# Performance work log

Measured on AMD Instinct MI355X. Metric: run time of the kernel, lower is better.

## Reference

```python
import jax, jax.numpy as jnp
import numpy as np
from jax import lax

H = 250  # hidden size of all LSTM layers


def _lstm_layer(x, Wih, Whh, bih, bhh):
    """Single-layer LSTM over time-major x [T, in], batch=1 folded away.
    PyTorch gate order: i, f, g, o. Returns hidden states [T, H]."""
    b = bih + bhh
    # Precompute input projections for all timesteps (parallel GEMM)
    xW = x @ Wih.T + b  # [T, 4H]

    def step(carry, xw_t):
        h, c = carry
        gates = xw_t + h @ Whh.T  # [4H]
        i, f, g, o = jnp.split(gates, 4)
        i = jax.nn.sigmoid(i)
        f = jax.nn.sigmoid(f)
        g = jnp.tanh(g)
        o = jax.nn.sigmoid(o)
        c = f * c + i * g
        h = o * jnp.tanh(c)
        return (h, c), h

    h0 = jnp.zeros((Whh.shape[1],), x.dtype)
    (_, _), hs = lax.scan(step, (h0, h0), xW)
    return hs  # [T, H]


def setup_inputs() -> dict:
    key = jax.random.key(0)
    ks = jax.random.split(key, 16)
    T, D = 8192, 1
    s = 1.0 / np.sqrt(H)  # PyTorch default uniform(-1/sqrt(H), 1/sqrt(H))
    u = lambda k, shape: jax.random.uniform(k, shape, jnp.float32, -s, s)
    inp = {
        "input_seq": jax.random.normal(ks[0], (T, D), jnp.float32),
        # lstm (2 layers), layer 0: input_size=1
        "Wih0": u(ks[1], (4 * H, D)), "Whh0": u(ks[2], (4 * H, H)),
        "bih0": u(ks[3], (4 * H,)), "bhh0": u(ks[4], (4 * H,)),
        # lstm layer 1: input=H
        "Wih1": u(ks[5], (4 * H, H)), "Whh1": u(ks[6], (4 * H, H)),
        "bih1": u(ks[7], (4 * H,)), "bhh1": u(ks[8], (4 * H,)),
        # lstm_1 (1 layer): input=H
        "Wih2": u(ks[9], (4 * H, H)), "Whh2": u(ks[10], (4 * H, H)),
        "bih2": u(ks[11], (4 * H,)), "bhh2": u(ks[12], (4 * H,)),
        # final linear H -> 1
        "Wl": u(ks[13], (1, H)), "bl": u(ks[14], (1,)),
    }
    return inp


def reference(input_seq, Wih0, Whh0, bih0, bhh0, Wih1, Whh1, bih1, bhh1,
              Wih2, Whh2, bih2, bhh2, Wl, bl):
    T = input_seq.shape[0]
    x = input_seq.reshape(T, -1)            # [T, 1] (batch=1 squeezed)
    h0 = _lstm_layer(x, Wih0, Whh0, bih0, bhh0)   # stacked LSTM layer 0
    h1 = _lstm_layer(h0, Wih1, Whh1, bih1, bhh1)  # layer 1 (dropout=0.2 inactive at eval)
    h2 = _lstm_layer(h1, Wih2, Whh2, bih2, bhh2)  # second LSTM module
    preds = h2 @ Wl.T + bl                  # [T, 1]
    return preds[-1]                        # [1]
```

## Files before the change

kernel.cpp:

```cpp
#include <hip/hip_runtime.h>
#include <cstdint>

#define HDIM 250
#define GDIM 1000
#define CH   64
#define PP   4
#define HRING 4
#define XRING 4
#define RPAD 1024
#define NTH  1024

#define LQ_N 8
#define LDSW_BYTES (LQ_N * NTH * 16)
#define HSEG 144
#define HBUF (4 * HSEG)
#define HB_BASE LDSW_BYTES
#define RED_BASE (HB_BASE + 2 * HBUF)
#define SMEM_BYTES (RED_BASE + 1024)

typedef _Float16 f16x2 __attribute__((ext_vector_type(2)));

__device__ __forceinline__ float fdot2u(uint32_t w, uint32_t h, float acc) {
#if defined(__has_builtin) && __has_builtin(__builtin_amdgcn_fdot2)
  return __builtin_amdgcn_fdot2(__builtin_bit_cast(f16x2, w),
                                __builtin_bit_cast(f16x2, h), acc, false);
#else
  f16x2 wv = __builtin_bit_cast(f16x2, w), hv = __builtin_bit_cast(f16x2, h);
  return acc + (float)wv[0] * (float)hv[0] + (float)wv[1] * (float)hv[1];
#endif
}

__device__ __forceinline__ uint32_t pkh2(float a, float b) {
  f16x2 p; p[0] = (_Float16)a; p[1] = (_Float16)b;
  return __builtin_bit_cast(uint32_t, p);
}

__device__ __forceinline__ uint4 pack8q(const float* rp, int c0) {
  float c[8];
#pragma unroll
  for (int u = 0; u < 8; ++u) {
    int col = c0 + u;
    c[u] = (rp && col < HDIM) ? rp[col] : 0.f;
  }
  uint4 r;
  r.x = pkh2(c[0], c[1]); r.y = pkh2(c[2], c[3]);
  r.z = pkh2(c[4], c[5]); r.w = pkh2(c[6], c[7]);
  return r;
}

__device__ __forceinline__ float rcpf_(float x) {
#if defined(__has_builtin) && __has_builtin(__builtin_amdgcn_rcpf)
  return __builtin_amdgcn_rcpf(x);
#else
  return 1.f / x;
#endif
}
__device__ __forceinline__ float sigm(float x) {
  return rcpf_(1.f + exp2f(-1.44269504088896341f * x));
}
__device__ __forceinline__ float tanh_(float x) {
  float e = exp2f(2.88539008177792681f * x);
  return 1.f - 2.f * rcpf_(e + 1.f);
}

template <int CTRL>
__device__ __forceinline__ float dppq(float v) {
  return __builtin_bit_cast(
      float, __builtin_amdgcn_update_dpp(0, __builtin_bit_cast(int, v), CTRL,
                                         0xF, 0xF, true));
}

__device__ __forceinline__ void step_barrier() {
  asm volatile("s_waitcnt lgkmcnt(0)\n\ts_barrier" ::: "memory");
}

#define F_HCNT(F, li)     (F)[(li)]
#define F_XWCON(F, li)    (F)[2 + (li)]
#define F_HDONE(F, li, p) (F)[4 + (li) * PP + (p)]
#define F_XWRDY(F, li, c) (F)[16 + (li) * 128 + (c)]

__device__ __forceinline__ int aload(int* p) {
  return __hip_atomic_load(p, __ATOMIC_RELAXED, __HIP_MEMORY_SCOPE_AGENT);
}
__device__ __forceinline__ void arel(int* p, int v) {
  __hip_atomic_store(p, v, __ATOMIC_RELEASE, __HIP_MEMORY_SCOPE_AGENT);
}
__device__ __forceinline__ void acq_fence() {
  __builtin_amdgcn_fence(__ATOMIC_ACQUIRE, "agent");
}
__device__ __forceinline__ void spin_ge(int* p, int tgt) {
  unsigned n = 0;
  while (aload(p) < tgt) {
    __builtin_amdgcn_s_sleep(2);
    if (++n > 200000000u) return;
  }
}

__global__ void lstm_init(const float* __restrict__ Wih1, const float* __restrict__ bih1,
                          const float* __restrict__ bhh1, const float* __restrict__ Wih2,
                          const float* __restrict__ bih2, const float* __restrict__ bhh2,
                          float* __restrict__ WT, float* __restrict__ BV) {
  int idx = blockIdx.x * blockDim.x + threadIdx.x;
  int stride = gridDim.x * blockDim.x;
  for (int i = idx; i < 2 * HDIM * RPAD; i += stride) {
    int li = i / (HDIM * RPAD);
    int rem = i - li * HDIM * RPAD;
    int j = rem / RPAD, r = rem - j * RPAD;
    const float* W = li ? Wih2 : Wih1;
    WT[i] = (r < GDIM) ? W[r * HDIM + j] : 0.f;
  }
  for (int i = idx; i < 2 * RPAD; i += stride) {
    int li = i >> 10, r = i & 1023;
    const float* bi = li ? bih2 : bih1;
    const float* bh = li ? bhh2 : bhh1;
    BV[i] = (r < GDIM) ? bi[r] + bh[r] : 0.f;
  }
}

__global__ void __launch_bounds__(NTH) lstm_main(
    const float* __restrict__ x, const float* __restrict__ Wih0,
    const float* __restrict__ bih0, const float* __restrict__ bhh0,
    const float* __restrict__ Whh0, const float* __restrict__ Whh1,
    const float* __restrict__ Whh2, const float* __restrict__ Wl,
    const float* __restrict__ bl, int* __restrict__ F,
    const float* __restrict__ WT, const float* __restrict__ BV,
    float* __restrict__ hRing, float* __restrict__ xwRing,
    float* __restrict__ out, int T) {
  __shared__ __align__(16) char smem[SMEM_BYTES];
  const int tid = threadIdx.x;
  const int bid = blockIdx.x;
  const int NC = T / CH;

  if (bid < 3) {
    const int L = bid;
    const int u = tid >> 2, sl = tid & 3;
    const bool uok = (u < HDIM);
    const int r_abs = sl * HDIM + u;

    const float* Whh = (L == 0) ? Whh0 : (L == 1) ? Whh1 : Whh2;
    char* lw = smem + tid * 16;
#define LWADDR(lq) (lw + (size_t)(lq) * (NTH * 16))
#define ROWP(r) (uok ? (Whh + ((size_t)(r) * HDIM + u) * HDIM) : (const float*)nullptr)

    uint4 w00, w01, w02, w03, w04, w05;
    uint4 w10, w11, w12, w13, w14, w15;
    uint4 w20, w21, w22, w23, w24, w25;
    uint4 w30, w31, w32, w33, w34, w35;
#define INITROW(r)                                          \
  w##r##0 = pack8q(ROWP(r), sl * 64 + 0);                   \
  w##r##1 = pack8q(ROWP(r), sl * 64 + 8);                   \
  w##r##2 = pack8q(ROWP(r), sl * 64 + 16);                  \
  w##r##3 = pack8q(ROWP(r), sl * 64 + 24);                  \
  w##r##4 = pack8q(ROWP(r), sl * 64 + 32);                  \
  w##r##5 = pack8q(ROWP(r), sl * 64 + 40);                  \
  *(uint4*)LWADDR(2 * (r)) = pack8q(ROWP(r), sl * 64 + 48); \
  *(uint4*)LWADDR(2 * (r) + 1) = pack8q(ROWP(r), sl * 64 + 56);
    INITROW(0) INITROW(1) INITROW(2) INITROW(3)

    float w0_ = 0.f, b0_ = 0.f;
    if (L == 0 && uok) {
      w0_ = Wih0[r_abs];
      b0_ = bih0[r_abs] + bhh0[r_abs];
    }

    for (int i = tid; i < (2 * HBUF) / 4; i += NTH)
      *(uint32_t*)(smem + HB_BASE + 4 * i) = 0u;
    __syncthreads();

    const float* xwBase = xwRing + (size_t)(L > 0 ? L - 1 : 0) * XRING * CH * RPAD;
    float* hBase = hRing + (size_t)L * HRING * CH * HDIM;
    float c_st = 0.f, h_last = 0.f;

    for (int tt = 0; tt < T; ++tt) {
      const int tc = tt & (CH - 1);
      const int c = tt >> 6;
      if (tc == 0) {
        if (tid == 0) {
          if (L > 0) spin_ge(&F_XWRDY(F, L - 1, c), 1);
          if (L < 2 && c >= HRING) {
            int cc = c - HRING;
            spin_ge(&F_HDONE(F, L, cc % PP), cc + 1);
          }
          acq_fence();
        }
        __syncthreads();
      }

      float xw = 0.f;
      if (uok) {
        if (L == 0) {
          xw = fmaf(x[tt], w0_, b0_);
        } else {
          const float* xp = xwBase + (size_t)(c & (XRING - 1)) * CH * RPAD +
                            (size_t)tc * RPAD;
          xw = xp[r_abs];
        }
      }

      const char* hb = smem + HB_BASE + (tt & 1) * HBUF + sl * HSEG;
      float a0 = 0.f, a1 = 0.f, a2 = 0.f, a3 = 0.f;
#define FD4(W_, H_, A_)                \
  A_ = fdot2u((W_).x, (H_).x, A_);     \
  A_ = fdot2u((W_).y, (H_).y, A_);     \
  A_ = fdot2u((W_).z, (H_).z, A_);     \
  A_ = fdot2u((W_).w, (H_).w, A_);
#define DOTK(k)                                      \
  {                                                  \
    const uint4 hq = *(const uint4*)(hb + (k) * 16); \
    FD4(w0##k, hq, a0)                               \
    FD4(w1##k, hq, a1)                               \
    FD4(w2##k, hq, a2)                               \
    FD4(w3##k, hq, a3)                               \
  }
      DOTK(0) DOTK(1) DOTK(2) DOTK(3) DOTK(4) DOTK(5)
      {
        const uint4 hq = *(const uint4*)(hb + 96);
        uint4 q;
        q = *(const uint4*)LWADDR(0); FD4(q, hq, a0)
        q = *(const uint4*)LWADDR(2); FD4(q, hq, a1)
        q = *(const uint4*)LWADDR(4); FD4(q, hq, a2)
        q = *(const uint4*)LWADDR(6); FD4(q, hq, a3)
      }
      {
        const uint4 hq = *(const uint4*)(hb + 112);
        uint4 q;
        q = *(const uint4*)LWADDR(1); FD4(q, hq, a0)
        q = *(const uint4*)LWADDR(3); FD4(q, hq, a1)
        q = *(const uint4*)LWADDR(5); FD4(q, hq, a2)
        q = *(const uint4*)LWADDR(7); FD4(q, hq, a3)
      }

      a0 += (sl == 0) ? xw : 0.f;
      a1 += (sl == 1) ? xw : 0.f;
      a2 += (sl == 2) ? xw : 0.f;
      a3 += (sl == 3) ? xw : 0.f;
      a0 += dppq<0xB1>(a0); a0 += dppq<0x4E>(a0);
      a1 += dppq<0xB1>(a1); a1 += dppq<0x4E>(a1);
      a2 += dppq<0xB1>(a2); a2 += dppq<0x4E>(a2);
      a3 += dppq<0xB1>(a3); a3 += dppq<0x4E>(a3);

      float ii = sigm(a0), ff = sigm(a1), tg = tanh_(a2), oo = sigm(a3);
      c_st = ff * c_st + ii * tg;
      float hn = oo * tanh_(c_st);
      h_last = hn;

      if (sl == 0 && uok) {
        char* hw = smem + HB_BASE + ((tt + 1) & 1) * HBUF + (u >> 6) * HSEG +
                   (u & 63) * 2;
        *(_Float16*)hw = (_Float16)hn;
        if (L < 2)
          hBase[(size_t)(c & (HRING - 1)) * CH * HDIM + (size_t)tc * HDIM + u] = hn;
      }

      if (tc == CH - 1) {
        __syncthreads();
        if (tid == 0) {
          if (L < 2) arel(&F_HCNT(F, L), c + 1);
          if (L > 0) arel(&F_XWCON(F, L - 1), c + 1);
        }
      } else {
        step_barrier();
      }
    }

    if (L == 2) {
      float* red = (float*)(smem + RED_BASE);
      if (sl == 0 && uok) red[u] = h_last;
      __syncthreads();
      if (tid == 0) {
        float s = bl[0];
        for (int j = 0; j < HDIM; ++j) s += red[j] * Wl[j];
        out[0] = s;
      }
    }
  } else {
    const int li = (bid - 3) / PP;
    const int p = (bid - 3) % PP;
    float* ldsH = (float*)smem;
    const int lane = tid & 63, wid = tid >> 6;
    const float* WTl = WT + (size_t)li * HDIM * RPAD;
    const float* BVl = BV + (size_t)li * RPAD;

    for (int c = p; c < NC; c += PP) {
      if (tid == 0) {
        spin_ge(&F_HCNT(F, li), c + 1);
        if (c >= XRING) spin_ge(&F_XWCON(F, li), c - XRING + 1);
        acq_fence();
      }
      __syncthreads();
      const float* hsrc = hRing + (size_t)li * HRING * CH * HDIM +
                          (size_t)(c & (HRING - 1)) * CH * HDIM;
      for (int t = wid; t < CH; t += 16)
        for (int j = lane; j < HDIM; j += 64)
          ldsH[t * 257 + j] = hsrc[t * HDIM + j];
      __syncthreads();
      if (tid == 0) arel(&F_HDONE(F, li, p), c + 1);

      float* xdst = xwRing + (size_t)li * XRING * CH * RPAD +
                    (size_t)(c & (XRING - 1)) * CH * RPAD;
      const int rb0 = wid * 64;
      for (int grpq = 0; grpq < 8; ++grpq) {
        const int rb = rb0 + grpq * 8;
        float acc[8];
#pragma unroll
        for (int uq = 0; uq < 8; ++uq) acc[uq] = 0.f;
        const float* wp = WTl + rb;
        float4 wa4 = *(const float4*)(wp);
        float4 wb4 = *(const float4*)(wp + 4);
        for (int j = 0; j < HDIM; ++j) {
          int jn = (j + 1 < HDIM) ? j + 1 : HDIM - 1;
          float4 na = *(const float4*)(wp + (size_t)jn * RPAD);
          float4 nb = *(const float4*)(wp + (size_t)jn * RPAD + 4);
          float hj = ldsH[lane * 257 + j];
          acc[0] = fmaf(wa4.x, hj, acc[0]); acc[1] = fmaf(wa4.y, hj, acc[1]);
          acc[2] = fmaf(wa4.z, hj, acc[2]); acc[3] = fmaf(wa4.w, hj, acc[3]);
          acc[4] = fmaf(wb4.x, hj, acc[4]); acc[5] = fmaf(wb4.y, hj, acc[5]);
          acc[6] = fmaf(wb4.z, hj, acc[6]); acc[7] = fmaf(wb4.w, hj, acc[7]);
          wa4 = na; wb4 = nb;
        }
#pragma unroll
        for (int uq = 0; uq < 8; ++uq) {
          int r = rb + uq;
          if (r < GDIM) xdst[(size_t)lane * RPAD + r] = acc[uq] + BVl[r];
        }
      }
      __syncthreads();
      if (tid == 0) arel(&F_XWRDY(F, li, c), 1);
    }
  }
}

extern "C" void kernel_launch(void* const* d_in, const int* in_sizes, int n_in,
                              void* d_out, int out_size, void* d_ws, size_t ws_size,
                              hipStream_t stream) {
  const float* x    = (const float*)d_in[0];
  const float* Wih0 = (const float*)d_in[1];
  const float* Whh0 = (const float*)d_in[2];
  const float* bih0 = (const float*)d_in[3];
  const float* bhh0 = (const float*)d_in[4];
  const float* Wih1 = (const float*)d_in[5];
  const float* Whh1 = (const float*)d_in[6];
  const float* bih1 = (const float*)d_in[7];
  const float* bhh1 = (const float*)d_in[8];
  const float* Wih2 = (const float*)d_in[9];
  const float* Whh2 = (const float*)d_in[10];
  const float* bih2 = (const float*)d_in[11];
  const float* bhh2 = (const float*)d_in[12];
  const float* Wl   = (const float*)d_in[13];
  const float* bl   = (const float*)d_in[14];
  const int T = in_sizes[0];

  char* ws = (char*)d_ws;
  int*   F   = (int*)ws;
  float* WT  = (float*)(ws + 4096);
  float* BV  = (float*)(ws + 4096 + 2048000);
  float* hR  = (float*)(ws + 4096 + 2048000 + 8192);
  float* xwR = (float*)(ws + 4096 + 2048000 + 8192 + 512000);

  hipMemsetAsync(F, 0, 4096, stream);
  lstm_init<<<256, 256, 0, stream>>>(Wih1, bih1, bhh1, Wih2, bih2, bhh2, WT, BV);
  lstm_main<<<3 + 2 * PP, NTH, 0, stream>>>(
      x, Wih0, bih0, bhh0, Whh0, Whh1, Whh2, Wl, bl, F, WT, BV, hR, xwR,
      (float*)d_out, T);
}
```

Measured before the change: 19.82 ms.

## Split each recurrent LSTM layer across four workgroups with cross-block hidden-state exchange

Each recurrent layer now runs on four workgroups, each owning a slice of about 64 hidden units with all four gate rows, instead of one workgroup per layer. This cuts per-step dot-product work and register and LDS weight storage per block. Hidden states are exchanged every timestep through global memory with per-block flags and spin-waits, and gates are gathered with ds_swizzle. The change trades per-step compute for a global-memory round trip and cross-CU synchronisation on the serial critical path, so latency could grow.

Measured after the change: 27.68 ms. +39.7%, slower.

```diff
diff --git a/kernel.cpp b/kernel.cpp
--- a/kernel.cpp
+++ b/kernel.cpp
@@ -5,18 +5,17 @@
 #define GDIM 1000
 #define CH   64
 #define PP   4
+#define NW   4
 #define HRING 4
 #define XRING 4
 #define RPAD 1024
 #define NTH  1024
 
-#define LQ_N 8
-#define LDSW_BYTES (LQ_N * NTH * 16)
 #define HSEG 144
 #define HBUF (4 * HSEG)
-#define HB_BASE LDSW_BYTES
+#define HB_BASE 32768
 #define RED_BASE (HB_BASE + 2 * HBUF)
-#define SMEM_BYTES (RED_BASE + 1024)
+#define SMEM_BYTES 92160
 
 typedef _Float16 f16x2 __attribute__((ext_vector_type(2)));
 
@@ -69,15 +68,21 @@
       float, __builtin_amdgcn_update_dpp(0, __builtin_bit_cast(int, v), CTRL,
                                          0xF, 0xF, true));
 }
+template <int IMM>
+__device__ __forceinline__ float swz(float v) {
+  return __builtin_bit_cast(
+      float, __builtin_amdgcn_ds_swizzle(__builtin_bit_cast(int, v), IMM));
+}
 
 __device__ __forceinline__ void step_barrier() {
   asm volatile("s_waitcnt lgkmcnt(0)\n\ts_barrier" ::: "memory");
 }
 
-#define F_HCNT(F, li)     (F)[(li)]
-#define F_XWCON(F, li)    (F)[2 + (li)]
-#define F_HDONE(F, li, p) (F)[4 + (li) * PP + (p)]
-#define F_XWRDY(F, li, c) (F)[16 + (li) * 128 + (c)]
+#define F_HCNTW(F, li, w)  (F)[(li) * 4 + (w)]
+#define F_XWCONW(F, li, w) (F)[8 + (li) * 4 + (w)]
+#define F_HDONE(F, li, p)  (F)[16 + (li) * 4 + (p)]
+#define F_XWRDY(F, li, c)  (F)[32 + (li) * 128 + (c)]
+#define F_HXC(F, L, w)     (F)[512 + (L) * 4 + (w)]
 
 __device__ __forceinline__ int aload(int* p) {
   return __hip_atomic_load(p, __ATOMIC_RELAXED, __HIP_MEMORY_SCOPE_AGENT);
@@ -92,7 +97,7 @@
   unsigned n = 0;
   while (aload(p) < tgt) {
     __builtin_amdgcn_s_sleep(2);
-    if (++n > 200000000u) return;
+    if (++n > 100000000u) return;
   }
 }
 
@@ -122,7 +127,7 @@
     const float* __restrict__ bih0, const float* __restrict__ bhh0,
     const float* __restrict__ Whh0, const float* __restrict__ Whh1,
     const float* __restrict__ Whh2, const float* __restrict__ Wl,
-    const float* __restrict__ bl, int* __restrict__ F,
+    const float* __restrict__ bl, int* __restrict__ F, float* __restrict__ hx,
     const float* __restrict__ WT, const float* __restrict__ BV,
     float* __restrict__ hRing, float* __restrict__ xwRing,
     float* __restrict__ out, int T) {
@@ -131,31 +136,30 @@
   const int bid = blockIdx.x;
   const int NC = T / CH;
 
-  if (bid < 3) {
-    const int L = bid;
-    const int u = tid >> 2, sl = tid & 3;
-    const bool uok = (u < HDIM);
-    const int r_abs = sl * HDIM + u;
+  if (bid < 12) {
+    const int L = bid >> 2, w = bid & 3;
+    const int sl = tid & 3;
+    const int gate = (tid >> 2) & 3;
+    const int lu = tid >> 4;
+    const int UW = (w < 3) ? 64 : 58;
+    const int u_glob = w * 64 + lu;
+    const bool uok = (lu < UW);
+    const bool lead = ((tid & 15) == 0) && uok;
+    const int r_abs = gate * HDIM + u_glob;
 
     const float* Whh = (L == 0) ? Whh0 : (L == 1) ? Whh1 : Whh2;
+    const float* rp = uok ? (Whh + (size_t)r_abs * HDIM) : (const float*)nullptr;
     char* lw = smem + tid * 16;
-#define LWADDR(lq) (lw + (size_t)(lq) * (NTH * 16))
-#define ROWP(r) (uok ? (Whh + ((size_t)(r) * HDIM + u) * HDIM) : (const float*)nullptr)
-
-    uint4 w00, w01, w02, w03, w04, w05;
-    uint4 w10, w11, w12, w13, w14, w15;
-    uint4 w20, w21, w22, w23, w24, w25;
-    uint4 w30, w31, w32, w33, w34, w35;
-#define INITROW(r)                                          \
-  w##r##0 = pack8q(ROWP(r), sl * 64 + 0);                   \
-  w##r##1 = pack8q(ROWP(r), sl * 64 + 8);                   \
-  w##r##2 = pack8q(ROWP(r), sl * 64 + 16);                  \
-  w##r##3 = pack8q(ROWP(r), sl * 64 + 24);                  \
-  w##r##4 = pack8q(ROWP(r), sl * 64 + 32);                  \
-  w##r##5 = pack8q(ROWP(r), sl * 64 + 40);                  \
-  *(uint4*)LWADDR(2 * (r)) = pack8q(ROWP(r), sl * 64 + 48); \
-  *(uint4*)LWADDR(2 * (r) + 1) = pack8q(ROWP(r), sl * 64 + 56);
-    INITROW(0) INITROW(1) INITROW(2) INITROW(3)
+#define LW(q) (lw + (size_t)(q) * (NTH * 16))
+
+    uint4 q0 = pack8q(rp, sl * 64 + 0);
+    uint4 q1 = pack8q(rp, sl * 64 + 8);
+    uint4 q2 = pack8q(rp, sl * 64 + 16);
+    uint4 q3 = pack8q(rp, sl * 64 + 24);
+    uint4 q4 = pack8q(rp, sl * 64 + 32);
+    uint4 q5 = pack8q(rp, sl * 64 + 40);
+    *(uint4*)LW(0) = pack8q(rp, sl * 64 + 48);
+    *(uint4*)LW(1) = pack8q(rp, sl * 64 + 56);
 
     float w0_ = 0.f, b0_ = 0.f;
     if (L == 0 && uok) {
@@ -163,17 +167,28 @@
       b0_ = bih0[r_abs] + bhh0[r_abs];
     }
 
+    const int lt = tid - 768;
+    int cw = -1, li2 = 0;
+    bool loader = false;
+    if (lt >= 0 && lt < 96) {
+      int idx = lt >> 5;
+      li2 = lt & 31;
+      cw = idx + (idx >= w ? 1 : 0);
+      loader = li2 < ((cw == 3) ? 29 : 32);
+    }
+
     for (int i = tid; i < (2 * HBUF) / 4; i += NTH)
       *(uint32_t*)(smem + HB_BASE + 4 * i) = 0u;
     __syncthreads();
 
     const float* xwBase = xwRing + (size_t)(L > 0 ? L - 1 : 0) * XRING * CH * RPAD;
     float* hBase = hRing + (size_t)L * HRING * CH * HDIM;
-    float c_st = 0.f, h_last = 0.f;
+    float c_st = 0.f;
 
     for (int tt = 0; tt < T; ++tt) {
       const int tc = tt & (CH - 1);
       const int c = tt >> 6;
+      const int p = tt & 1, ns = p ^ 1;
       if (tc == 0) {
         if (tid == 0) {
           if (L > 0) spin_ge(&F_XWRDY(F, L - 1, c), 1);
@@ -197,85 +212,86 @@
         }
       }
 
-      const char* hb = smem + HB_BASE + (tt & 1) * HBUF + sl * HSEG;
-      float a0 = 0.f, a1 = 0.f, a2 = 0.f, a3 = 0.f;
-#define FD4(W_, H_, A_)                \
-  A_ = fdot2u((W_).x, (H_).x, A_);     \
-  A_ = fdot2u((W_).y, (H_).y, A_);     \
-  A_ = fdot2u((W_).z, (H_).z, A_);     \
-  A_ = fdot2u((W_).w, (H_).w, A_);
-#define DOTK(k)                                      \
-  {                                                  \
-    const uint4 hq = *(const uint4*)(hb + (k) * 16); \
-    FD4(w0##k, hq, a0)                               \
-    FD4(w1##k, hq, a1)                               \
-    FD4(w2##k, hq, a2)                               \
-    FD4(w3##k, hq, a3)                               \
-  }
-      DOTK(0) DOTK(1) DOTK(2) DOTK(3) DOTK(4) DOTK(5)
-      {
-        const uint4 hq = *(const uint4*)(hb + 96);
-        uint4 q;
-        q = *(const uint4*)LWADDR(0); FD4(q, hq, a0)
-        q = *(const uint4*)LWADDR(2); FD4(q, hq, a1)
-        q = *(const uint4*)LWADDR(4); FD4(q, hq, a2)
-        q = *(const uint4*)LWADDR(6); FD4(q, hq, a3)
-      }
-      {
-        const uint4 hq = *(const uint4*)(hb + 112);
-        uint4 q;
-        q = *(const uint4*)LWADDR(1); FD4(q, hq, a0)
-        q = *(const uint4*)LWADDR(3); FD4(q, hq, a1)
-        q = *(const uint4*)LWADDR(5); FD4(q, hq, a2)
-        q = *(const uint4*)LWADDR(7); FD4(q, hq, a3)
-      }
-
-      a0 += (sl == 0) ? xw : 0.f;
-      a1 += (sl == 1) ? xw : 0.f;
-      a2 += (sl == 2) ? xw : 0.f;
-      a3 += (sl == 3) ? xw : 0.f;
-      a0 += dppq<0xB1>(a0); a0 += dppq<0x4E>(a0);
-      a1 += dppq<0xB1>(a1); a1 += dppq<0x4E>(a1);
-      a2 += dppq<0xB1>(a2); a2 += dppq<0x4E>(a2);
-      a3 += dppq<0xB1>(a3); a3 += dppq<0x4E>(a3);
-
-      float ii = sigm(a0), ff = sigm(a1), tg = tanh_(a2), oo = sigm(a3);
+      const char* hbp = smem + HB_BASE + p * HBUF + sl * HSEG;
+      float a = 0.f;
+#define FD4(W_, H_)                  \
+  a = fdot2u((W_).x, (H_).x, a);     \
+  a = fdot2u((W_).y, (H_).y, a);     \
+  a = fdot2u((W_).z, (H_).z, a);     \
+  a = fdot2u((W_).w, (H_).w, a);
+      { uint4 hq = *(const uint4*)(hbp + 0);  FD4(q0, hq) }
+      { uint4 hq = *(const uint4*)(hbp + 16); FD4(q1, hq) }
+      { uint4 hq = *(const uint4*)(hbp + 32); FD4(q2, hq) }
+      { uint4 hq = *(const uint4*)(hbp + 48); FD4(q3, hq) }
+      { uint4 hq = *(const uint4*)(hbp + 64); FD4(q4, hq) }
+      { uint4 hq = *(const uint4*)(hbp + 80); FD4(q5, hq) }
+      { uint4 hq = *(const uint4*)(hbp + 96);  uint4 t6 = *(const uint4*)LW(0); FD4(t6, hq) }
+      { uint4 hq = *(const uint4*)(hbp + 112); uint4 t7 = *(const uint4*)LW(1); FD4(t7, hq) }
+
+      a += dppq<0xB1>(a);
+      a += dppq<0x4E>(a);
+      a += xw;
+
+      float v4 = swz<0x101F>(a);
+      float v8 = swz<0x201F>(a);
+      float vc = swz<0x301F>(a);
+      const float gi = (gate == 0) ? a : (gate == 1) ? v4 : (gate == 2) ? v8 : vc;
+      const float gf = ((gate ^ 1) == 0) ? a : ((gate ^ 1) == 1) ? v4 : ((gate ^ 1) == 2) ? v8 : vc;
+      const float gG = ((gate ^ 2) == 0) ? a : ((gate ^ 2) == 1) ? v4 : ((gate ^ 2) == 2) ? v8 : vc;
+      const float go = ((gate ^ 3) == 0) ? a : ((gate ^ 3) == 1) ? v4 : ((gate ^ 3) == 2) ? v8 : vc;
+
+      const float ii = sigm(gi), ff = sigm(gf), tg = tanh_(gG), oo = sigm(go);
       c_st = ff * c_st + ii * tg;
-      float hn = oo * tanh_(c_st);
-      h_last = hn;
-
-      if (sl == 0 && uok) {
-        char* hw = smem + HB_BASE + ((tt + 1) & 1) * HBUF + (u >> 6) * HSEG +
-                   (u & 63) * 2;
-        *(_Float16*)hw = (_Float16)hn;
+      const float hn = oo * tanh_(c_st);
+
+      if (lead) {
         if (L < 2)
-          hBase[(size_t)(c & (HRING - 1)) * CH * HDIM + (size_t)tc * HDIM + u] = hn;
-      }
-
-      if (tc == CH - 1) {
-        __syncthreads();
-        if (tid == 0) {
-          if (L < 2) arel(&F_HCNT(F, L), c + 1);
-          if (L > 0) arel(&F_XWCON(F, L - 1), c + 1);
-        }
-      } else {
-        step_barrier();
-      }
-    }
-
-    if (L == 2) {
+          hBase[(size_t)(c & (HRING - 1)) * CH * HDIM + (size_t)tc * HDIM + u_glob] = hn;
+        __hip_atomic_store((uint32_t*)&hx[(L * 2 + ns) * 256 + u_glob],
+                           __builtin_bit_cast(uint32_t, hn), __ATOMIC_RELAXED,
+                           __HIP_MEMORY_SCOPE_AGENT);
+      }
+      asm volatile("s_waitcnt vmcnt(0)" ::: "memory");
+      __syncthreads();
+      if (tid == 0) {
+        arel(&F_HXC(F, L, w), tt + 1);
+        if (tc == CH - 1) {
+          if (L < 2) arel(&F_HCNTW(F, L, w), c + 1);
+          if (L > 0) arel(&F_XWCONW(F, L - 1, w), c + 1);
+        }
+      }
+
+      if (lead)
+        *(_Float16*)(smem + HB_BASE + ns * HBUF + (u_glob >> 6) * HSEG +
+                     (u_glob & 63) * 2) = (_Float16)hn;
+      if (loader) {
+        spin_ge(&F_HXC(F, L, cw), tt + 1);
+        acq_fence();
+        const float2 hv = *(const float2*)&hx[(L * 2 + ns) * 256 + 64 * cw + 2 * li2];
+        *(uint32_t*)(smem + HB_BASE + ns * HBUF + cw * HSEG + 4 * li2) =
+            pkh2(hv.x, hv.y);
+      }
+      step_barrier();
+    }
+
+    if (L == 2 && w == 0) {
       float* red = (float*)(smem + RED_BASE);
-      if (sl == 0 && uok) red[u] = h_last;
+      const int pT = T & 1;
+      if (tid < HDIM) {
+        float hv = (float)*(_Float16*)(smem + HB_BASE + pT * HBUF +
+                                       (tid >> 6) * HSEG + (tid & 63) * 2);
+        red[tid] = hv * Wl[tid];
+      }
       __syncthreads();
       if (tid == 0) {
         float s = bl[0];
-        for (int j = 0; j < HDIM; ++j) s += red[j] * Wl[j];
+        for (int j = 0; j < HDIM; ++j) s += red[j];
         out[0] = s;
       }
     }
   } else {
-    const int li = (bid - 3) / PP;
-    const int p = (bid - 3) % PP;
+    const int li = (bid - 12) / PP;
+    const int p = (bid - 12) % PP;
     float* ldsH = (float*)smem;
     const int lane = tid & 63, wid = tid >> 6;
     const float* WTl = WT + (size_t)li * HDIM * RPAD;
@@ -283,8 +299,10 @@
 
     for (int c = p; c < NC; c += PP) {
       if (tid == 0) {
-        spin_ge(&F_HCNT(F, li), c + 1);
-        if (c >= XRING) spin_ge(&F_XWCON(F, li), c - XRING + 1);
+        for (int ww = 0; ww < NW; ++ww) spin_ge(&F_HCNTW(F, li, ww), c + 1);
+        if (c >= XRING)
+          for (int ww = 0; ww < NW; ++ww)
+            spin_ge(&F_XWCONW(F, li, ww), c - XRING + 1);
         acq_fence();
       }
       __syncthreads();
@@ -352,14 +370,15 @@
 
   char* ws = (char*)d_ws;
   int*   F   = (int*)ws;
-  float* WT  = (float*)(ws + 4096);
-  float* BV  = (float*)(ws + 4096 + 2048000);
-  float* hR  = (float*)(ws + 4096 + 2048000 + 8192);
-  float* xwR = (float*)(ws + 4096 + 2048000 + 8192 + 512000);
-
-  hipMemsetAsync(F, 0, 4096, stream);
+  float* hx  = (float*)(ws + 4096);
+  float* WT  = (float*)(ws + 12288);
+  float* BV  = (float*)(ws + 12288 + 2048000);
+  float* hR  = (float*)(ws + 12288 + 2048000 + 8192);
+  float* xwR = (float*)(ws + 12288 + 2048000 + 8192 + 512000);
+
+  hipMemsetAsync(ws, 0, 12288, stream);
   lstm_init<<<256, 256, 0, stream>>>(Wih1, bih1, bhh1, Wih2, bih2, bhh2, WT, BV);
-  lstm_main<<<3 + 2 * PP, NTH, 0, stream>>>(
-      x, Wih0, bih0, bhh0, Whh0, Whh1, Whh2, Wl, bl, F, WT, BV, hR, xwR,
+  lstm_main<<<12 + 2 * PP, NTH, 0, stream>>>(
+      x, Wih0, bih0, bhh0, Whh0, Whh1, Whh2, Wl, bl, F, hx, WT, BV, hR, xwR,
       (float*)d_out, T);
 }
```

## Use one thread per hidden unit with weights split across registers, LDS and streamed global memory

Applied to the files above, without the earlier changes.

The recurrent blocks drop from 1024 threads with 4-way K-splitting and DPP reductions to 256 threads, each computing all four gates of one hidden unit over the full K. The Whh rows are split three ways: the first 80 columns stay in registers, the next 72 sit in LDS, and the rest are pre-packed by the init kernel into a global buffer streamed every step, interleaved with compute. This removes the cross-lane reductions and shrinks the barrier scope. In exchange each step does more serial work per thread and depends on per-step global or L2 loads. Ring depths are halved, spin sleep and timeout are reduced, and the projection blocks are resized to the new thread count.

Result: slower. 47.74 ms (+140.9%).

```diff
diff --git a/kernel.cpp b/kernel.cpp
--- a/kernel.cpp
+++ b/kernel.cpp
@@ -5,17 +5,15 @@
 #define GDIM 1000
 #define CH   64
 #define PP   4
-#define HRING 4
-#define XRING 4
+#define HRING 2
+#define XRING 2
 #define RPAD 1024
-#define NTH  1024
-
-#define LQ_N 8
-#define LDSW_BYTES (LQ_N * NTH * 16)
-#define HSEG 144
-#define HBUF (4 * HSEG)
+#define NTH  256
+
+#define NSTR 52
+#define LDSW_BYTES (36 * NTH * 16)
 #define HB_BASE LDSW_BYTES
-#define RED_BASE (HB_BASE + 2 * HBUF)
+#define RED_BASE (HB_BASE + 1024)
 #define SMEM_BYTES (RED_BASE + 1024)
 
 typedef _Float16 f16x2 __attribute__((ext_vector_type(2)));
@@ -63,13 +61,6 @@
   return 1.f - 2.f * rcpf_(e + 1.f);
 }
 
-template <int CTRL>
-__device__ __forceinline__ float dppq(float v) {
-  return __builtin_bit_cast(
-      float, __builtin_amdgcn_update_dpp(0, __builtin_bit_cast(int, v), CTRL,
-                                         0xF, 0xF, true));
-}
-
 __device__ __forceinline__ void step_barrier() {
   asm volatile("s_waitcnt lgkmcnt(0)\n\ts_barrier" ::: "memory");
 }
@@ -91,15 +82,17 @@
 __device__ __forceinline__ void spin_ge(int* p, int tgt) {
   unsigned n = 0;
   while (aload(p) < tgt) {
-    __builtin_amdgcn_s_sleep(2);
-    if (++n > 200000000u) return;
+    __builtin_amdgcn_s_sleep(1);
+    if (++n > 20000000u) return;
   }
 }
 
 __global__ void lstm_init(const float* __restrict__ Wih1, const float* __restrict__ bih1,
                           const float* __restrict__ bhh1, const float* __restrict__ Wih2,
                           const float* __restrict__ bih2, const float* __restrict__ bhh2,
-                          float* __restrict__ WT, float* __restrict__ BV) {
+                          const float* __restrict__ Whh0, const float* __restrict__ Whh1,
+                          const float* __restrict__ Whh2, float* __restrict__ WT,
+                          float* __restrict__ BV, uint4* __restrict__ sbuf) {
   int idx = blockIdx.x * blockDim.x + threadIdx.x;
   int stride = gridDim.x * blockDim.x;
   for (int i = idx; i < 2 * HDIM * RPAD; i += stride) {
@@ -115,6 +108,16 @@
     const float* bh = li ? bhh2 : bhh1;
     BV[i] = (r < GDIM) ? bi[r] + bh[r] : 0.f;
   }
+  for (int i = idx; i < 3 * NSTR * NTH; i += stride) {
+    int L = i / (NSTR * NTH);
+    int r2 = i - L * (NSTR * NTH);
+    int q = r2 / NTH, t = r2 % NTH;
+    int k = 19 + (q >> 2), g = q & 3;
+    const float* W = (L == 0) ? Whh0 : (L == 1) ? Whh1 : Whh2;
+    const float* rp =
+        (t < HDIM) ? (W + ((size_t)(g * HDIM + t)) * HDIM) : (const float*)nullptr;
+    sbuf[(size_t)L * NSTR * NTH + q * NTH + t] = pack8q(rp, k * 8);
+  }
 }
 
 __global__ void __launch_bounds__(NTH) lstm_main(
@@ -123,9 +126,9 @@
     const float* __restrict__ Whh0, const float* __restrict__ Whh1,
     const float* __restrict__ Whh2, const float* __restrict__ Wl,
     const float* __restrict__ bl, int* __restrict__ F,
-    const float* __restrict__ WT, const float* __restrict__ BV,
-    float* __restrict__ hRing, float* __restrict__ xwRing,
-    float* __restrict__ out, int T) {
+    const uint4* __restrict__ sbuf, const float* __restrict__ WT,
+    const float* __restrict__ BV, float* __restrict__ hRing,
+    float* __restrict__ xwRing, float* __restrict__ out, int T) {
   __shared__ __align__(16) char smem[SMEM_BYTES];
   const int tid = threadIdx.x;
   const int bid = blockIdx.x;
@@ -133,40 +136,42 @@
 
   if (bid < 3) {
     const int L = bid;
-    const int u = tid >> 2, sl = tid & 3;
+    const int u = tid;
     const bool uok = (u < HDIM);
-    const int r_abs = sl * HDIM + u;
 
     const float* Whh = (L == 0) ? Whh0 : (L == 1) ? Whh1 : Whh2;
-    char* lw = smem + tid * 16;
-#define LWADDR(lq) (lw + (size_t)(lq) * (NTH * 16))
-#define ROWP(r) (uok ? (Whh + ((size_t)(r) * HDIM + u) * HDIM) : (const float*)nullptr)
-
-    uint4 w00, w01, w02, w03, w04, w05;
-    uint4 w10, w11, w12, w13, w14, w15;
-    uint4 w20, w21, w22, w23, w24, w25;
-    uint4 w30, w31, w32, w33, w34, w35;
-#define INITROW(r)                                          \
-  w##r##0 = pack8q(ROWP(r), sl * 64 + 0);                   \
-  w##r##1 = pack8q(ROWP(r), sl * 64 + 8);                   \
-  w##r##2 = pack8q(ROWP(r), sl * 64 + 16);                  \
-  w##r##3 = pack8q(ROWP(r), sl * 64 + 24);                  \
-  w##r##4 = pack8q(ROWP(r), sl * 64 + 32);                  \
-  w##r##5 = pack8q(ROWP(r), sl * 64 + 40);                  \
-  *(uint4*)LWADDR(2 * (r)) = pack8q(ROWP(r), sl * 64 + 48); \
-  *(uint4*)LWADDR(2 * (r) + 1) = pack8q(ROWP(r), sl * 64 + 56);
-    INITROW(0) INITROW(1) INITROW(2) INITROW(3)
-
-    float w0_ = 0.f, b0_ = 0.f;
+#define RPg(g) (uok ? (Whh + ((size_t)((g) * HDIM + u)) * HDIM) : (const float*)nullptr)
+
+    uint4 w0_0, w0_1, w0_2, w0_3, w0_4, w0_5, w0_6, w0_7, w0_8, w0_9;
+    uint4 w1_0, w1_1, w1_2, w1_3, w1_4, w1_5, w1_6, w1_7, w1_8, w1_9;
+    uint4 w2_0, w2_1, w2_2, w2_3, w2_4, w2_5, w2_6, w2_7, w2_8, w2_9;
+    uint4 w3_0, w3_1, w3_2, w3_3, w3_4, w3_5, w3_6, w3_7, w3_8, w3_9;
+#define INITG(g)                                                      \
+  w##g##_0 = pack8q(RPg(g), 0);  w##g##_1 = pack8q(RPg(g), 8);        \
+  w##g##_2 = pack8q(RPg(g), 16); w##g##_3 = pack8q(RPg(g), 24);       \
+  w##g##_4 = pack8q(RPg(g), 32); w##g##_5 = pack8q(RPg(g), 40);       \
+  w##g##_6 = pack8q(RPg(g), 48); w##g##_7 = pack8q(RPg(g), 56);       \
+  w##g##_8 = pack8q(RPg(g), 64); w##g##_9 = pack8q(RPg(g), 72);
+    INITG(0) INITG(1) INITG(2) INITG(3)
+
+    for (int g = 0; g < 4; ++g)
+      for (int k = 10; k < 19; ++k)
+        *(uint4*)(smem + (size_t)((((k - 10) * 4 + g) * NTH) + tid) * 16) =
+            pack8q(RPg(g), k * 8);
+
+    float w0g0 = 0.f, w0g1 = 0.f, w0g2 = 0.f, w0g3 = 0.f;
+    float b0g0 = 0.f, b0g1 = 0.f, b0g2 = 0.f, b0g3 = 0.f;
     if (L == 0 && uok) {
-      w0_ = Wih0[r_abs];
-      b0_ = bih0[r_abs] + bhh0[r_abs];
+      w0g0 = Wih0[u];           b0g0 = bih0[u] + bhh0[u];
+      w0g1 = Wih0[HDIM + u];    b0g1 = bih0[HDIM + u] + bhh0[HDIM + u];
+      w0g2 = Wih0[2*HDIM + u];  b0g2 = bih0[2*HDIM + u] + bhh0[2*HDIM + u];
+      w0g3 = Wih0[3*HDIM + u];  b0g3 = bih0[3*HDIM + u] + bhh0[3*HDIM + u];
     }
 
-    for (int i = tid; i < (2 * HBUF) / 4; i += NTH)
-      *(uint32_t*)(smem + HB_BASE + 4 * i) = 0u;
+    if (tid < 128) ((uint2*)(smem + HB_BASE))[tid] = make_uint2(0u, 0u);
     __syncthreads();
 
+    const uint4* sp = sbuf + (size_t)L * NSTR * NTH + tid;
     const float* xwBase = xwRing + (size_t)(L > 0 ? L - 1 : 0) * XRING * CH * RPAD;
     float* hBase = hRing + (size_t)L * HRING * CH * HDIM;
     float c_st = 0.f, h_last = 0.f;
@@ -174,90 +179,102 @@
     for (int tt = 0; tt < T; ++tt) {
       const int tc = tt & (CH - 1);
       const int c = tt >> 6;
+      const int p = tt & 1, ns = p ^ 1;
       if (tc == 0) {
         if (tid == 0) {
           if (L > 0) spin_ge(&F_XWRDY(F, L - 1, c), 1);
-          if (L < 2 && c >= HRING) {
-            int cc = c - HRING;
-            spin_ge(&F_HDONE(F, L, cc % PP), cc + 1);
-          }
+          if (L < 2 && c >= HRING)
+            spin_ge(&F_HDONE(F, L, (c - HRING) % PP), c - HRING + 1);
           acq_fence();
         }
         __syncthreads();
       }
 
-      float xw = 0.f;
-      if (uok) {
-        if (L == 0) {
-          xw = fmaf(x[tt], w0_, b0_);
-        } else {
-          const float* xp = xwBase + (size_t)(c & (XRING - 1)) * CH * RPAD +
-                            (size_t)tc * RPAD;
-          xw = xp[r_abs];
-        }
-      }
-
-      const char* hb = smem + HB_BASE + (tt & 1) * HBUF + sl * HSEG;
+      float xw0, xw1, xw2, xw3;
+      if (L == 0) {
+        float xt = x[tt];
+        xw0 = fmaf(xt, w0g0, b0g0); xw1 = fmaf(xt, w0g1, b0g1);
+        xw2 = fmaf(xt, w0g2, b0g2); xw3 = fmaf(xt, w0g3, b0g3);
+      } else {
+        const float* xp = xwBase + (size_t)(c & (XRING - 1)) * CH * RPAD +
+                          (size_t)tc * RPAD;
+        xw0 = xp[u]; xw1 = xp[HDIM + u]; xw2 = xp[2*HDIM + u]; xw3 = xp[3*HDIM + u];
+      }
+
+      const uint4* hb = (const uint4*)(smem + HB_BASE + p * 512);
       float a0 = 0.f, a1 = 0.f, a2 = 0.f, a3 = 0.f;
+
 #define FD4(W_, H_, A_)                \
   A_ = fdot2u((W_).x, (H_).x, A_);     \
   A_ = fdot2u((W_).y, (H_).y, A_);     \
   A_ = fdot2u((W_).z, (H_).z, A_);     \
   A_ = fdot2u((W_).w, (H_).w, A_);
-#define DOTK(k)                                      \
-  {                                                  \
-    const uint4 hq = *(const uint4*)(hb + (k) * 16); \
-    FD4(w0##k, hq, a0)                               \
-    FD4(w1##k, hq, a1)                               \
-    FD4(w2##k, hq, a2)                               \
-    FD4(w3##k, hq, a3)                               \
-  }
-      DOTK(0) DOTK(1) DOTK(2) DOTK(3) DOTK(4) DOTK(5)
-      {
-        const uint4 hq = *(const uint4*)(hb + 96);
-        uint4 q;
-        q = *(const uint4*)LWADDR(0); FD4(q, hq, a0)
-        q = *(const uint4*)LWADDR(2); FD4(q, hq, a1)
-        q = *(const uint4*)LWADDR(4); FD4(q, hq, a2)
-        q = *(const uint4*)LWADDR(6); FD4(q, hq, a3)
-      }
-      {
-        const uint4 hq = *(const uint4*)(hb + 112);
-        uint4 q;
-        q = *(const uint4*)LWADDR(1); FD4(q, hq, a0)
-        q = *(const uint4*)LWADDR(3); FD4(q, hq, a1)
-        q = *(const uint4*)LWADDR(5); FD4(q, hq, a2)
-        q = *(const uint4*)LWADDR(7); FD4(q, hq, a3)
-      }
-
-      a0 += (sl == 0) ? xw : 0.f;
-      a1 += (sl == 1) ? xw : 0.f;
-      a2 += (sl == 2) ? xw : 0.f;
-      a3 += (sl == 3) ? xw : 0.f;
-      a0 += dppq<0xB1>(a0); a0 += dppq<0x4E>(a0);
-      a1 += dppq<0xB1>(a1); a1 += dppq<0x4E>(a1);
-      a2 += dppq<0xB1>(a2); a2 += dppq<0x4E>(a2);
-      a3 += dppq<0xB1>(a3); a3 += dppq<0x4E>(a3);
-
-      float ii = sigm(a0), ff = sigm(a1), tg = tanh_(a2), oo = sigm(a3);
+#define LDR(r)                                      \
+  const uint4 s##r##_0 = sp[((r) * 4 + 0) * NTH],   \
+              s##r##_1 = sp[((r) * 4 + 1) * NTH],   \
+              s##r##_2 = sp[((r) * 4 + 2) * NTH],   \
+              s##r##_3 = sp[((r) * 4 + 3) * NTH];
+#define CONS(r)                                     \
+  {                                                 \
+    const uint4 hq = hb[19 + (r)];                  \
+    FD4(s##r##_0, hq, a0) FD4(s##r##_1, hq, a1)     \
+    FD4(s##r##_2, hq, a2) FD4(s##r##_3, hq, a3)     \
+  }
+#define DOTREG(k)                                   \
+  {                                                 \
+    const uint4 hq = hb[k];                         \
+    FD4(w0_##k, hq, a0) FD4(w1_##k, hq, a1)         \
+    FD4(w2_##k, hq, a2) FD4(w3_##k, hq, a3)         \
+  }
+#define DOTLDS(k)                                                            \
+  {                                                                          \
+    const uint4 hq = hb[k];                                                  \
+    uint4 t0 = *(const uint4*)(smem + (size_t)(((((k)-10) * 4 + 0) * NTH) + tid) * 16); \
+    FD4(t0, hq, a0)                                                          \
+    uint4 t1 = *(const uint4*)(smem + (size_t)(((((k)-10) * 4 + 1) * NTH) + tid) * 16); \
+    FD4(t1, hq, a1)                                                          \
+    uint4 t2 = *(const uint4*)(smem + (size_t)(((((k)-10) * 4 + 2) * NTH) + tid) * 16); \
+    FD4(t2, hq, a2)                                                          \
+    uint4 t3 = *(const uint4*)(smem + (size_t)(((((k)-10) * 4 + 3) * NTH) + tid) * 16); \
+    FD4(t3, hq, a3)                                                          \
+  }
+
+      LDR(0) LDR(1)
+      DOTREG(0) DOTREG(1)
+      LDR(2) DOTREG(2) DOTREG(3)
+      CONS(0) LDR(3) DOTREG(4) DOTREG(5)
+      CONS(1) LDR(4) DOTREG(6) DOTREG(7)
+      CONS(2) LDR(5) DOTREG(8) DOTREG(9)
+      CONS(3) LDR(6) DOTLDS(10) DOTLDS(11)
+      CONS(4) LDR(7) DOTLDS(12) DOTLDS(13)
+      CONS(5) LDR(8) DOTLDS(14) DOTLDS(15)
+      CONS(6) LDR(9) DOTLDS(16) DOTLDS(17)
+      CONS(7) LDR(10) DOTLDS(18)
+      CONS(8) LDR(11)
+      CONS(9) LDR(12)
+      CONS(10) CONS(11) CONS(12)
+
+      a0 += xw0; a1 += xw1; a2 += xw2; a3 += xw3;
+
+      const float ii = sigm(a0), ff = sigm(a1), tg = tanh_(a2), oo = sigm(a3);
       c_st = ff * c_st + ii * tg;
-      float hn = oo * tanh_(c_st);
+      const float hn = oo * tanh_(c_st);
       h_last = hn;
 
-      if (sl == 0 && uok) {
-        char* hw = smem + HB_BASE + ((tt + 1) & 1) * HBUF + (u >> 6) * HSEG +
-                   (u & 63) * 2;
-        *(_Float16*)hw = (_Float16)hn;
+      if (uok) {
+        *(_Float16*)(smem + HB_BASE + ns * 512 + u * 2) = (_Float16)hn;
         if (L < 2)
           hBase[(size_t)(c & (HRING - 1)) * CH * HDIM + (size_t)tc * HDIM + u] = hn;
       }
 
       if (tc == CH - 1) {
+        asm volatile("s_waitcnt vmcnt(0)" ::: "memory");
         __syncthreads();
         if (tid == 0) {
           if (L < 2) arel(&F_HCNT(F, L), c + 1);
           if (L > 0) arel(&F_XWCON(F, L - 1), c + 1);
         }
+        __syncthreads();
       } else {
         step_barrier();
       }
@@ -265,11 +282,11 @@
 
     if (L == 2) {
       float* red = (float*)(smem + RED_BASE);
-      if (sl == 0 && uok) red[u] = h_last;
+      if (uok) red[u] = h_last * Wl[u];
       __syncthreads();
       if (tid == 0) {
         float s = bl[0];
-        for (int j = 0; j < HDIM; ++j) s += red[j] * Wl[j];
+        for (int j = 0; j < HDIM; ++j) s += red[j];
         out[0] = s;
       }
     }
@@ -290,7 +307,7 @@
       __syncthreads();
       const float* hsrc = hRing + (size_t)li * HRING * CH * HDIM +
                           (size_t)(c & (HRING - 1)) * CH * HDIM;
-      for (int t = wid; t < CH; t += 16)
+      for (int t = wid; t < CH; t += 4)
         for (int j = lane; j < HDIM; j += 64)
           ldsH[t * 257 + j] = hsrc[t * HDIM + j];
       __syncthreads();
@@ -298,8 +315,8 @@
 
       float* xdst = xwRing + (size_t)li * XRING * CH * RPAD +
                     (size_t)(c & (XRING - 1)) * CH * RPAD;
-      const int rb0 = wid * 64;
-      for (int grpq = 0; grpq < 8; ++grpq) {
+      const int rb0 = wid * 256;
+      for (int grpq = 0; grpq < 32; ++grpq) {
         const int rb = rb0 + grpq * 8;
         float acc[8];
 #pragma unroll
@@ -351,15 +368,17 @@
   const int T = in_sizes[0];
 
   char* ws = (char*)d_ws;
-  int*   F   = (int*)ws;
-  float* WT  = (float*)(ws + 4096);
-  float* BV  = (float*)(ws + 4096 + 2048000);
-  float* hR  = (float*)(ws + 4096 + 2048000 + 8192);
-  float* xwR = (float*)(ws + 4096 + 2048000 + 8192 + 512000);
+  int*   F    = (int*)ws;
+  float* WT   = (float*)(ws + 4096);
+  float* BV   = (float*)(ws + 2052096);
+  uint4* sbuf = (uint4*)(ws + 2060288);
+  float* hR   = (float*)(ws + 2699264);
+  float* xwR  = (float*)(ws + 2955264);
 
   hipMemsetAsync(F, 0, 4096, stream);
-  lstm_init<<<256, 256, 0, stream>>>(Wih1, bih1, bhh1, Wih2, bih2, bhh2, WT, BV);
+  lstm_init<<<256, 256, 0, stream>>>(Wih1, bih1, bhh1, Wih2, bih2, bhh2,
+                                     Whh0, Whh1, Whh2, WT, BV, sbuf);
   lstm_main<<<3 + 2 * PP, NTH, 0, stream>>>(
-      x, Wih0, bih0, bhh0, Whh0, Whh1, Whh2, Wl, bl, F, WT, BV, hR, xwR,
+      x, Wih0, bih0, bhh0, Whh0, Whh1, Whh2, Wl, bl, F, sbuf, WT, BV, hR, xwR,
       (float*)d_out, T);
 }
```

## Stage most recurrent weights in AGPRs via inline asm, shrink VGPR pressure

Applied to the files above, without the earlier changes.

Moves most per-thread Whh fp16 weight slices from VGPRs into accumulation registers (AGPRs) using v_accvgpr_write/read inline asm, keeps only two chunks per gate in VGPRs, and spills one extra chunk into LDS (LQ_N 8→9). The intent is to relieve VGPR pressure in the 1024-thread recurrent loop, avoiding spills or allowing better scheduling, while keeping weights on-chip. It also shortens the spin-wait sleep and timeout. The cost is an extra accvgpr_read before each dot2, plus one more LDS read per step, on the serial critical path.

Result: slower. 20.78 ms (+4.8%).

```diff
diff --git a/kernel.cpp b/kernel.cpp
--- a/kernel.cpp
+++ b/kernel.cpp
@@ -10,7 +10,7 @@
 #define RPAD 1024
 #define NTH  1024
 
-#define LQ_N 8
+#define LQ_N 9
 #define LDSW_BYTES (LQ_N * NTH * 16)
 #define HSEG 144
 #define HBUF (4 * HSEG)
@@ -74,6 +74,9 @@
   asm volatile("s_waitcnt lgkmcnt(0)\n\ts_barrier" ::: "memory");
 }
 
+#define AWR(dst, src) \
+  asm volatile("v_accvgpr_write_b32 %0, %1" : "=a"(dst) : "v"(src))
+
 #define F_HCNT(F, li)     (F)[(li)]
 #define F_XWCON(F, li)    (F)[2 + (li)]
 #define F_HDONE(F, li, p) (F)[4 + (li) * PP + (p)]
@@ -91,8 +94,8 @@
 __device__ __forceinline__ void spin_ge(int* p, int tgt) {
   unsigned n = 0;
   while (aload(p) < tgt) {
-    __builtin_amdgcn_s_sleep(2);
-    if (++n > 200000000u) return;
+    __builtin_amdgcn_s_sleep(1);
+    if (++n > 100000000u) return;
   }
 }
 
@@ -139,23 +142,41 @@
 
     const float* Whh = (L == 0) ? Whh0 : (L == 1) ? Whh1 : Whh2;
     char* lw = smem + tid * 16;
-#define LWADDR(lq) (lw + (size_t)(lq) * (NTH * 16))
+#define LWADDR(s) (lw + (size_t)(s) * (NTH * 16))
 #define ROWP(r) (uok ? (Whh + ((size_t)(r) * HDIM + u) * HDIM) : (const float*)nullptr)
 
-    uint4 w00, w01, w02, w03, w04, w05;
-    uint4 w10, w11, w12, w13, w14, w15;
-    uint4 w20, w21, w22, w23, w24, w25;
-    uint4 w30, w31, w32, w33, w34, w35;
-#define INITROW(r)                                          \
-  w##r##0 = pack8q(ROWP(r), sl * 64 + 0);                   \
-  w##r##1 = pack8q(ROWP(r), sl * 64 + 8);                   \
-  w##r##2 = pack8q(ROWP(r), sl * 64 + 16);                  \
-  w##r##3 = pack8q(ROWP(r), sl * 64 + 24);                  \
-  w##r##4 = pack8q(ROWP(r), sl * 64 + 32);                  \
-  w##r##5 = pack8q(ROWP(r), sl * 64 + 40);                  \
-  *(uint4*)LWADDR(2 * (r)) = pack8q(ROWP(r), sl * 64 + 48); \
-  *(uint4*)LWADDR(2 * (r) + 1) = pack8q(ROWP(r), sl * 64 + 56);
-    INITROW(0) INITROW(1) INITROW(2) INITROW(3)
+    uint4 w00, w01, w10, w11, w20, w21, w30, w31;
+    w00 = pack8q(ROWP(0), sl * 64 + 0); w01 = pack8q(ROWP(0), sl * 64 + 8);
+    w10 = pack8q(ROWP(1), sl * 64 + 0); w11 = pack8q(ROWP(1), sl * 64 + 8);
+    w20 = pack8q(ROWP(2), sl * 64 + 0); w21 = pack8q(ROWP(2), sl * 64 + 8);
+    w30 = pack8q(ROWP(3), sl * 64 + 0); w31 = pack8q(ROWP(3), sl * 64 + 8);
+
+#define DECLAQ(r, k) \
+  uint32_t ag##r##_##k##_0, ag##r##_##k##_1, ag##r##_##k##_2, ag##r##_##k##_3;
+    DECLAQ(0, 2) DECLAQ(0, 3) DECLAQ(0, 4) DECLAQ(0, 5)
+    DECLAQ(1, 2) DECLAQ(1, 3) DECLAQ(1, 4) DECLAQ(1, 5)
+    DECLAQ(2, 2) DECLAQ(2, 3) DECLAQ(2, 4) DECLAQ(2, 5)
+    DECLAQ(3, 2) DECLAQ(3, 3) DECLAQ(3, 4)
+#define IAQ(r, k)                                               \
+  {                                                             \
+    uint4 q = pack8q(ROWP(r), sl * 64 + (k) * 8);               \
+    AWR(ag##r##_##k##_0, q.x); AWR(ag##r##_##k##_1, q.y);       \
+    AWR(ag##r##_##k##_2, q.z); AWR(ag##r##_##k##_3, q.w);       \
+  }
+    IAQ(0, 2) IAQ(0, 3) IAQ(0, 4) IAQ(0, 5)
+    IAQ(1, 2) IAQ(1, 3) IAQ(1, 4) IAQ(1, 5)
+    IAQ(2, 2) IAQ(2, 3) IAQ(2, 4) IAQ(2, 5)
+    IAQ(3, 2) IAQ(3, 3) IAQ(3, 4)
+
+    *(uint4*)LWADDR(0) = pack8q(ROWP(0), sl * 64 + 48);
+    *(uint4*)LWADDR(1) = pack8q(ROWP(0), sl * 64 + 56);
+    *(uint4*)LWADDR(2) = pack8q(ROWP(1), sl * 64 + 48);
+    *(uint4*)LWADDR(3) = pack8q(ROWP(1), sl * 64 + 56);
+    *(uint4*)LWADDR(4) = pack8q(ROWP(2), sl * 64 + 48);
+    *(uint4*)LWADDR(5) = pack8q(ROWP(2), sl * 64 + 56);
+    *(uint4*)LWADDR(6) = pack8q(ROWP(3), sl * 64 + 40);
+    *(uint4*)LWADDR(7) = pack8q(ROWP(3), sl * 64 + 48);
+    *(uint4*)LWADDR(8) = pack8q(ROWP(3), sl * 64 + 56);
 
     float w0_ = 0.f, b0_ = 0.f;
     if (L == 0 && uok) {
@@ -199,35 +220,70 @@
 
       const char* hb = smem + HB_BASE + (tt & 1) * HBUF + sl * HSEG;
       float a0 = 0.f, a1 = 0.f, a2 = 0.f, a3 = 0.f;
+
 #define FD4(W_, H_, A_)                \
   A_ = fdot2u((W_).x, (H_).x, A_);     \
   A_ = fdot2u((W_).y, (H_).y, A_);     \
   A_ = fdot2u((W_).z, (H_).z, A_);     \
   A_ = fdot2u((W_).w, (H_).w, A_);
-#define DOTK(k)                                      \
-  {                                                  \
-    const uint4 hq = *(const uint4*)(hb + (k) * 16); \
-    FD4(w0##k, hq, a0)                               \
-    FD4(w1##k, hq, a1)                               \
-    FD4(w2##k, hq, a2)                               \
-    FD4(w3##k, hq, a3)                               \
-  }
-      DOTK(0) DOTK(1) DOTK(2) DOTK(3) DOTK(4) DOTK(5)
+#define AQ(r, k, A_)                                                      \
+  asm("v_accvgpr_read_b32 %1, %5\n\t"                                     \
+      "v_accvgpr_read_b32 %2, %6\n\t"                                     \
+      "v_accvgpr_read_b32 %3, %7\n\t"                                     \
+      "v_accvgpr_read_b32 %4, %8\n\t"                                     \
+      "v_dot2_f32_f16 %0, %1, %9, %0\n\t"                                 \
+      "v_dot2_f32_f16 %0, %2, %10, %0\n\t"                                \
+      "v_dot2_f32_f16 %0, %3, %11, %0\n\t"                                \
+      "v_dot2_f32_f16 %0, %4, %12, %0"                                    \
+      : "+v"(A_), "=&v"(q0_), "=&v"(q1_), "=&v"(q2_), "=&v"(q3_)          \
+      : "a"(ag##r##_##k##_0), "a"(ag##r##_##k##_1), "a"(ag##r##_##k##_2), \
+        "a"(ag##r##_##k##_3), "v"(hq.x), "v"(hq.y), "v"(hq.z), "v"(hq.w))
+
+      {
+        const uint4 hq = *(const uint4*)(hb + 0);
+        FD4(w00, hq, a0) FD4(w10, hq, a1) FD4(w20, hq, a2) FD4(w30, hq, a3)
+      }
+      {
+        const uint4 hq = *(const uint4*)(hb + 16);
+        FD4(w01, hq, a0) FD4(w11, hq, a1) FD4(w21, hq, a2) FD4(w31, hq, a3)
+      }
+      {
+        const uint4 hq = *(const uint4*)(hb + 32);
+        uint32_t q0_, q1_, q2_, q3_;
+        AQ(0, 2, a0); AQ(1, 2, a1); AQ(2, 2, a2); AQ(3, 2, a3);
+      }
+      {
+        const uint4 hq = *(const uint4*)(hb + 48);
+        uint32_t q0_, q1_, q2_, q3_;
+        AQ(0, 3, a0); AQ(1, 3, a1); AQ(2, 3, a2); AQ(3, 3, a3);
+      }
+      {
+        const uint4 hq = *(const uint4*)(hb + 64);
+        uint32_t q0_, q1_, q2_, q3_;
+        AQ(0, 4, a0); AQ(1, 4, a1); AQ(2, 4, a2); AQ(3, 4, a3);
+      }
+      {
+        const uint4 hq = *(const uint4*)(hb + 80);
+        uint32_t q0_, q1_, q2_, q3_;
+        AQ(0, 5, a0); AQ(1, 5, a1); AQ(2, 5, a2);
+        uint4 t = *(const uint4*)LWADDR(6);
+        FD4(t, hq, a3)
+      }
       {
         const uint4 hq = *(const uint4*)(hb + 96);
-        uint4 q;
-        q = *(const uint4*)LWADDR(0); FD4(q, hq, a0)
-        q = *(const uint4*)LWADDR(2); FD4(q, hq, a1)
-        q = *(const uint4*)LWADDR(4); FD4(q, hq, a2)
-        q = *(const uint4*)LWADDR(6); FD4(q, hq, a3)
+        uint4 t;
+        t = *(const uint4*)LWADDR(0); FD4(t, hq, a0)
+        t = *(const uint4*)LWADDR(2); FD4(t, hq, a1)
+        t = *(const uint4*)LWADDR(4); FD4(t, hq, a2)
+        t = *(const uint4*)LWADDR(7); FD4(t, hq, a3)
       }
       {
         const uint4 hq = *(const uint4*)(hb + 112);
-        uint4 q;
-        q = *(const uint4*)LWADDR(1); FD4(q, hq, a0)
-        q = *(const uint4*)LWADDR(3); FD4(q, hq, a1)
-        q = *(const uint4*)LWADDR(5); FD4(q, hq, a2)
-        q = *(const uint4*)LWADDR(7); FD4(q, hq, a3)
+        uint4 t;
+        t = *(const uint4*)LWADDR(1); FD4(t, hq, a0)
+        t = *(const uint4*)LWADDR(3); FD4(t, hq, a1)
+        t = *(const uint4*)LWADDR(5); FD4(t, hq, a2)
+        t = *(const uint4*)LWADDR(8); FD4(t, hq, a3)
       }
 
       a0 += (sl == 0) ? xw : 0.f;
```
